# Kernel tuning notes

Measured on AMD Instinct MI355X. Metric: run time of the kernel, lower is better.

Reference implementation:

```python
import jax, jax.numpy as jnp
import numpy as np

HIDDEN = 2048
INTER = 4096
HEADS = 32
HEAD_DIM = INTER // HEADS  # 128
STATE = 128
GROUPS = 1
CONV_K = 4
CHUNK = 256
EPS = 1e-5
CONV_DIM = INTER + 2 * GROUPS * STATE  # 4352
DT_MIN, DT_MAX = 0.0, 100.0
BATCH, SEQ = 2, 4096


def _segment_sum(x):
    """Stable segment sum: returns (..., T, T) with entry [i,j] = sum_{k=j+1..i} x[k] (-inf above diag)."""
    T = x.shape[-1]
    xx = jnp.broadcast_to(x[..., None], x.shape + (T,))
    mask_lower = jnp.tril(jnp.ones((T, T), bool), -1)
    xx = jnp.where(mask_lower, xx, 0.0)
    seg = jnp.cumsum(xx, axis=-2)
    mask_incl = jnp.tril(jnp.ones((T, T), bool), 0)
    return jnp.where(mask_incl, seg, -jnp.inf)


def setup_inputs() -> dict:
    key = jax.random.key(0)
    ks = jax.random.split(key, 8)
    std = 0.02
    return {
        "hidden_states": jax.random.normal(ks[0], (BATCH, SEQ, HIDDEN), jnp.float32),
        "in_proj_w": jax.random.normal(ks[1], (INTER + CONV_DIM + HEADS, HIDDEN), jnp.float32) * std,
        "conv_w": jax.random.normal(ks[2], (CONV_DIM, 1, CONV_K), jnp.float32) * std,
        "conv_b": jnp.zeros((CONV_DIM,), jnp.float32),
        "A_log": jnp.log(jax.random.uniform(ks[3], (HEADS,), jnp.float32, 1.0, 16.0)),
        "dt_bias": jax.random.normal(ks[4], (HEADS,), jnp.float32) * 0.1,
        "D": jnp.ones((HEADS,), jnp.float32),
        "norm_w": jnp.ones((INTER,), jnp.float32),
        "out_proj_w": jax.random.normal(ks[5], (HIDDEN, INTER), jnp.float32) * (std / np.sqrt(48.0)),
    }


def reference(hidden_states, in_proj_w, conv_w, conv_b, A_log, dt_bias, D, norm_w, out_proj_w):
    b, s, _ = hidden_states.shape
    # in_proj and split into gate / conv-input / dt
    proj = hidden_states @ in_proj_w.T
    gate, hBC, dt = jnp.split(proj, [INTER, INTER + CONV_DIM], axis=-1)

    # causal depthwise conv1d (padding k-1 left, truncate to seq_len) + SiLU
    x = jnp.transpose(hBC, (0, 2, 1))  # (b, conv_dim, s)
    x = jax.lax.conv_general_dilated(
        x, conv_w, window_strides=(1,), padding=[(CONV_K - 1, 0)],
        dimension_numbers=("NCH", "OIH", "NCH"), feature_group_count=CONV_DIM)
    x = x + conv_b[None, :, None]
    hBC = jax.nn.silu(jnp.transpose(x, (0, 2, 1)))  # (b, s, conv_dim)

    xs, B, C = jnp.split(hBC, [INTER, INTER + GROUPS * STATE], axis=-1)

    A = -jnp.exp(A_log)  # (h,)
    dt = jnp.clip(jax.nn.softplus(dt + dt_bias), DT_MIN, DT_MAX)  # (b, s, h)

    xs = xs.reshape(b, s, HEADS, HEAD_DIM)
    rep = HEADS // GROUPS
    Bm = jnp.repeat(B.reshape(b, s, GROUPS, STATE), rep, axis=2)  # (b,s,h,n)
    Cm = jnp.repeat(C.reshape(b, s, GROUPS, STATE), rep, axis=2)

    pad = (-s) % CHUNK

    def padseq(t):
        return jnp.pad(t, ((0, 0), (0, pad)) + ((0, 0),) * (t.ndim - 2))

    D_res = D[None, None, :, None] * padseq(xs)  # (b, S, h, p)
    xdt = padseq(xs * dt[..., None])
    Ad = padseq(A[None, None, :] * dt)  # (b, S, h)
    Bm, Cm = padseq(Bm), padseq(Cm)

    nc = (s + pad) // CHUNK
    xdt = xdt.reshape(b, nc, CHUNK, HEADS, HEAD_DIM)
    Ad = jnp.transpose(Ad.reshape(b, nc, CHUNK, HEADS), (0, 3, 1, 2))  # (b,h,c,l)
    Bm = Bm.reshape(b, nc, CHUNK, HEADS, STATE)
    Cm = Cm.reshape(b, nc, CHUNK, HEADS, STATE)

    A_cum = jnp.cumsum(Ad, axis=-1)  # (b,h,c,l)

    # 1) intra-chunk (diagonal block) output
    L = jnp.exp(_segment_sum(Ad))  # (b,h,c,l,l)
    G = jnp.einsum("bclhn,bcshn->bclsh", Cm, Bm)
    M = G * jnp.transpose(L, (0, 2, 3, 4, 1))
    Y_diag = jnp.einsum("bclsh,bcshp->bclhp", M, xdt)

    # 2) per-chunk final states
    decay_states = jnp.exp(A_cum[:, :, :, -1:] - A_cum)  # (b,h,c,l)
    B_decay = Bm * jnp.transpose(decay_states, (0, 2, 3, 1))[..., None]
    states = jnp.einsum("bclhn,bclhp->bchpn", B_decay, xdt)  # (b,c,h,p,n)

    # 3) inter-chunk recurrence
    states = jnp.concatenate([jnp.zeros_like(states[:, :1]), states], axis=1)  # (b,c+1,h,p,n)
    chunk_sums = jnp.pad(A_cum[:, :, :, -1], ((0, 0), (0, 0), (1, 0)))  # (b,h,c+1)
    decay_chunk = jnp.exp(_segment_sum(chunk_sums))  # (b,h,c+1,c+1)
    decay_chunk = jnp.transpose(decay_chunk, (0, 2, 3, 1))  # (b,c,z,h)
    new_states = jnp.einsum("bczh,bchpn->bzhpn", decay_chunk, states)
    states = new_states[:, :-1]  # (b,c,h,p,n) state entering each chunk

    # 4) state -> output contribution
    state_decay = jnp.exp(A_cum)  # (b,h,c,l)
    Y_off = jnp.einsum("bclhn,bchpn->bclhp", Cm, states) * jnp.transpose(state_decay, (0, 2, 3, 1))[..., None]

    y = (Y_diag + Y_off).reshape(b, nc * CHUNK, HEADS, HEAD_DIM) + D_res
    y = y[:, :s].reshape(b, s, INTER)

    # gated RMSNorm
    y = y * jax.nn.silu(gate)
    var = jnp.mean(y * y, axis=-1, keepdims=True)
    y = y * jax.lax.rsqrt(var + EPS) * norm_w

    return y @ out_proj_w.T
```

## Files before the change

### kernel.cpp

```cpp
#include <hip/hip_runtime.h>

#define SEQ     4096
#define BATCH   2
#define NROWS   8192
#define HID     2048
#define INTER_  4096
#define NHEADS  32
#define HDIM    128
#define NSTATE  128
#define CDIM    4352
#define NPROJ_  8480
#define NPAD    8704
#define NCH     16
#define CHUNK_  256

typedef __attribute__((ext_vector_type(8))) short bf16x8;
typedef __attribute__((ext_vector_type(4))) short short4v;
typedef __attribute__((ext_vector_type(4))) float f32x4;

#define AS1 __attribute__((address_space(1)))
#define AS3 __attribute__((address_space(3)))

__device__ __forceinline__ float bf2f(short s) {
  union { unsigned u; float f; } x;
  x.u = ((unsigned)(unsigned short)s) << 16;
  return x.f;
}
__device__ __forceinline__ short f2bf(float f) {
  union { float f; unsigned u; } x; x.f = f;
  unsigned r = x.u + 0x7FFFu + ((x.u >> 16) & 1u);
  return (short)(r >> 16);
}

__global__ void cvt_bf16(const float* __restrict__ in, short* __restrict__ out,
                         int n4, int nsrc4) {
  int i = blockIdx.x * 256 + threadIdx.x;
  if (i >= n4) return;
  short4v o = {0, 0, 0, 0};
  if (i < nsrc4) {
    f32x4 v = *(const f32x4*)(in + (size_t)i * 4);
    o = (short4v){ f2bf(v.x), f2bf(v.y), f2bf(v.z), f2bf(v.w) };
  }
  *(short4v*)(out + (size_t)i * 4) = o;
}

template<int MODE>
__global__ __launch_bounds__(512, 1)
void gemm256(const short* __restrict__ A, const short* __restrict__ Bw,
             int M, int N, int K, int nM,
             float* __restrict__ outF, short* __restrict__ gate,
             short* __restrict__ hbc, float* __restrict__ dtraw)
{
  __shared__ __align__(16) short lds[2][2][2][256 * 32];
  const int tid = threadIdx.x;
  const int lane = tid & 63, wave = tid >> 6;
  const int l16 = lane & 15, lhi = lane >> 4;
  const int wm = wave >> 2, wn = wave & 3;

  const int bm = blockIdx.x % nM, bn = blockIdx.x / nM;
  const size_t row0 = (size_t)bm * 256;
  const int    col0 = bn * 256;

  const short* Ab  = A + row0 * K;
  const short* Bbp = Bw + (size_t)col0 * K;

  f32x4 acc[8][4];
  #pragma unroll
  for (int m = 0; m < 8; ++m)
    #pragma unroll
    for (int n = 0; n < 4; ++n) acc[m][n] = (f32x4){0.f, 0.f, 0.f, 0.f};

  auto stage = [&](int bufq, int mat, int kh, int ko) {
    const short* gsrc = mat ? Bbp : Ab;
    short* base = &lds[bufq][mat][kh][0];
    #pragma unroll
    for (int j = 0; j < 2; ++j) {
      int u = j * 512 + tid;
      int r = u >> 2;
      int g = (u & 3) ^ ((r >> 1) & 3);
      __builtin_amdgcn_global_load_lds(
          (const AS1 unsigned*)(gsrc + (size_t)r * K + ko + kh * 32 + g * 8),
          (AS3 unsigned*)(base + (j * 512 + wave * 64) * 8), 16, 0, 0);
    }
  };
  auto readA = [&](int bufq, int kh, int mh, bf16x8* a) {
    const short* base = &lds[bufq][0][kh][0];
    #pragma unroll
    for (int f = 0; f < 4; ++f) {
      int rr = wm * 128 + mh * 64 + f * 16 + l16;
      int g = lhi ^ ((rr >> 1) & 3);
      a[f] = *(const bf16x8*)(base + rr * 32 + g * 8);
    }
  };
  auto readB = [&](int bufq, int kh, bf16x8* b) {
    const short* base = &lds[bufq][1][kh][0];
    #pragma unroll
    for (int f = 0; f < 4; ++f) {
      int rr = wn * 64 + f * 16 + l16;
      int g = lhi ^ ((rr >> 1) & 3);
      b[f] = *(const bf16x8*)(base + rr * 32 + g * 8);
    }
  };

  const int nt = K / 64;
  stage(0, 0, 0, 0); stage(0, 1, 0, 0); stage(0, 0, 1, 0); stage(0, 1, 1, 0);

  for (int t = 0; t < nt; ++t) {
    const int buf = t & 1, nb = buf ^ 1;
    const int kon = (t + 1) * 64;
    const bool pf = (t + 1 < nt);

    if (pf) { stage(nb, 0, 0, kon); stage(nb, 1, 0, kon);
              stage(nb, 0, 1, kon); stage(nb, 1, 1, kon); }
    if (pf) asm volatile("s_waitcnt vmcnt(8)" ::: "memory");
    else    asm volatile("s_waitcnt vmcnt(0)" ::: "memory");
    __builtin_amdgcn_s_barrier();

    #pragma unroll
    for (int kh = 0; kh < 2; ++kh) {
      bf16x8 a[8], b[4];
      readA(buf, kh, 0, a); readA(buf, kh, 1, a + 4); readB(buf, kh, b);
      __builtin_amdgcn_s_setprio(1);
      #pragma unroll
      for (int mf = 0; mf < 8; ++mf)
        #pragma unroll
        for (int nf = 0; nf < 4; ++nf)
          acc[mf][nf] = __builtin_amdgcn_mfma_f32_16x16x32_bf16(a[mf], b[nf], acc[mf][nf], 0, 0, 0);
      __builtin_amdgcn_s_setprio(0);
    }
    __builtin_amdgcn_s_barrier();
  }

  #pragma unroll
  for (int mh = 0; mh < 2; ++mh) {
    #pragma unroll
    for (int f = 0; f < 4; ++f) {
      #pragma unroll
      for (int nf = 0; nf < 4; ++nf) {
        #pragma unroll
        for (int j = 0; j < 4; ++j) {
          int gr = (int)row0 + wm * 128 + mh * 64 + f * 16 + lhi * 4 + j;
          int gc = col0 + wn * 64 + nf * 16 + l16;
          float v = acc[mh * 4 + f][nf][j];
          if (MODE == 0) {
            outF[(size_t)gr * N + gc] = v;
          } else {
            if (gc < INTER_)             gate[(size_t)gr * INTER_ + gc] = f2bf(v);
            else if (gc < INTER_ + CDIM) hbc[(size_t)gr * CDIM + (gc - INTER_)] = f2bf(v);
            else if (gc < NPROJ_)        dtraw[(size_t)gr * NHEADS + (gc - INTER_ - CDIM)] = v;
          }
        }
      }
    }
  }
}

__global__ __launch_bounds__(256)
void conv_t(const short* __restrict__ hbc, const float* __restrict__ cw,
            const float* __restrict__ cb, short* __restrict__ xsT,
            short* __restrict__ Bb, short* __restrict__ Cb, short* __restrict__ BbT)
{
  __shared__ short sOut[64][130];
  int ct = blockIdx.y;
  int cl = threadIdx.x & 127;
  int rh = threadIdx.x >> 7;
  int c = ct * 128 + cl;
  int row0 = blockIdx.x * 64;
  int s0 = row0 & (SEQ - 1);
  float w0 = cw[c * 4 + 0], w1 = cw[c * 4 + 1], w2 = cw[c * 4 + 2], w3 = cw[c * 4 + 3];
  float bias = cb[c];
  int r0 = rh * 32;
  float h0, h1, h2;
  h0 = (s0 + r0 - 3 >= 0) ? bf2f(hbc[(size_t)(row0 + r0 - 3) * CDIM + c]) : 0.f;
  h1 = (s0 + r0 - 2 >= 0) ? bf2f(hbc[(size_t)(row0 + r0 - 2) * CDIM + c]) : 0.f;
  h2 = (s0 + r0 - 1 >= 0) ? bf2f(hbc[(size_t)(row0 + r0 - 1) * CDIM + c]) : 0.f;

  for (int r = r0; r < r0 + 32; ++r) {
    float xin = bf2f(hbc[(size_t)(row0 + r) * CDIM + c]);
    float a = bias + w0 * h0 + w1 * h1 + w2 * h2 + w3 * xin;
    h0 = h1; h1 = h2; h2 = xin;
    float v = a / (1.f + expf(-a));
    short bv = f2bf(v);
    if (ct < 33) sOut[r][cl] = bv;
    if (ct == 32)      Bb[(size_t)(row0 + r) * NSTATE + cl] = bv;
    else if (ct == 33) Cb[(size_t)(row0 + r) * NSTATE + cl] = bv;
  }
  if (ct >= 33) return;
  __syncthreads();
  int p = threadIdx.x >> 1, sh = (threadIdx.x & 1) * 32;
  int b = row0 >> 12;
  size_t dst;
  short* outp;
  if (ct < 32) { outp = xsT; dst = ((size_t)(b * 32 + ct) * 128 + p) * SEQ + s0 + sh; }
  else         { outp = BbT; dst = ((size_t)b * 128 + p) * SEQ + s0 + sh; }
  #pragma unroll
  for (int g = 0; g < 8; ++g) {
    short4v o;
    o[0] = sOut[sh + g * 4 + 0][p];
    o[1] = sOut[sh + g * 4 + 1][p];
    o[2] = sOut[sh + g * 4 + 2][p];
    o[3] = sOut[sh + g * 4 + 3][p];
    *(short4v*)(outp + dst + g * 4) = o;
  }
}

__global__ void dt_proc(const float* __restrict__ dtraw, const float* __restrict__ dtb,
                        float* __restrict__ dtT, int n) {
  int i = blockIdx.x * 256 + threadIdx.x;
  if (i >= n) return;
  float x = dtraw[i] + dtb[i & (NHEADS - 1)];
  float sp = (x > 20.f) ? x : log1pf(expf(x));
  float d = fminf(fmaxf(sp, 0.f), 100.f);
  int row = i >> 5, h = i & 31;
  dtT[(size_t)h * NROWS + row] = d;
}

__global__ __launch_bounds__(256)
void ssm_state(const short* __restrict__ xsT, const short* __restrict__ BbT,
               const float* __restrict__ dtT, const float* __restrict__ Alog,
               short* __restrict__ csb, float* __restrict__ dAsum)
{
  int blk = blockIdx.x;
  int h = blk & 31, cc = (blk >> 5) & 15, b = blk >> 9;
  int tid = threadIdx.x, lane = tid & 63, wave = tid >> 6;
  int l16 = lane & 15, lhi = lane >> 4;
  int s0 = cc * CHUNK_;

  __shared__ float acum[256];
  __shared__ float sdt[256];
  { float Ah = -expf(Alog[h]);
    float d = dtT[(size_t)h * NROWS + (size_t)b * SEQ + s0 + tid];
    sdt[tid] = d; acum[tid] = Ah * d; }
  for (int off = 1; off < 256; off <<= 1) {
    __syncthreads();
    float v = (tid >= off) ? acum[tid - off] : 0.f;
    __syncthreads();
    acum[tid] += v;
  }
  __syncthreads();
  float alast = acum[255];

  const short* xbase = xsT + ((size_t)(b * 32 + h) * 128) * SEQ + s0;
  const short* bbase = BbT + ((size_t)b * 128) * SEQ + s0;

  f32x4 acc[2][8];
  #pragma unroll
  for (int m = 0; m < 2; ++m)
    #pragma unroll
    for (int n = 0; n < 8; ++n) acc[m][n] = (f32x4){0.f, 0.f, 0.f, 0.f};

  for (int lt0 = 0; lt0 < 256; lt0 += 32) {
    float fe[8];
    #pragma unroll
    for (int e = 0; e < 8; ++e) {
      int kl = lt0 + lhi * 8 + e;
      fe[e] = sdt[kl] * __expf(alast - acum[kl]);
    }
    bf16x8 af[2];
    #pragma unroll
    for (int m = 0; m < 2; ++m) {
      bf16x8 raw = *(const bf16x8*)(xbase + (size_t)(wave * 32 + m * 16 + l16) * SEQ + lt0 + lhi * 8);
      bf16x8 sc;
      #pragma unroll
      for (int e = 0; e < 8; ++e) sc[e] = f2bf(bf2f(raw[e]) * fe[e]);
      af[m] = sc;
    }
    #pragma unroll
    for (int n = 0; n < 8; ++n) {
      bf16x8 bfv = *(const bf16x8*)(bbase + (size_t)(n * 16 + l16) * SEQ + lt0 + lhi * 8);
      acc[0][n] = __builtin_amdgcn_mfma_f32_16x16x32_bf16(af[0], bfv, acc[0][n], 0, 0, 0);
      acc[1][n] = __builtin_amdgcn_mfma_f32_16x16x32_bf16(af[1], bfv, acc[1][n], 0, 0, 0);
    }
  }
  size_t base = (size_t)blk * 16384;
  #pragma unroll
  for (int m = 0; m < 2; ++m)
    #pragma unroll
    for (int n = 0; n < 8; ++n)
      #pragma unroll
      for (int j = 0; j < 4; ++j) {
        int p = wave * 32 + m * 16 + lhi * 4 + j;
        int ng = n * 16 + l16;
        csb[base + (size_t)p * NSTATE + ng] = f2bf(acc[m][n][j]);
      }
  if (tid == 0) dAsum[blk] = alast;
}

__global__ void ssm_scan(short* __restrict__ csb, const float* __restrict__ dAsum) {
  int idx = blockIdx.x * 256 + threadIdx.x;
  int np = idx & 16383;
  int bh = idx >> 14;
  int h = bh & 31, b = bh >> 5;
  float run = 0.f;
  #pragma unroll
  for (int c = 0; c < NCH; ++c) {
    size_t base = ((size_t)((b * NCH + c) * NHEADS + h)) * 16384 + np;
    float v = bf2f(csb[base]);
    csb[base] = f2bf(run);
    run = run * __expf(dAsum[(b * NCH + c) * NHEADS + h]) + v;
  }
}

__global__ __launch_bounds__(256)
void ssm_y(const short* __restrict__ xsT, const short* __restrict__ Bb,
           const short* __restrict__ Cb, const float* __restrict__ dtT,
           const float* __restrict__ Alog, const float* __restrict__ Dv,
           const short* __restrict__ csb, short* __restrict__ gateY)
{
  int blk = blockIdx.y, lt = blockIdx.x;
  int h = blk & 31, cc = (blk >> 5) & 15, b = blk >> 9;
  int tid = threadIdx.x, lane = tid & 63, wave = tid >> 6;
  int l16 = lane & 15, lhi = lane >> 4;
  int s0 = cc * CHUNK_;
  size_t row0 = (size_t)b * SEQ + s0;

  __shared__ float acum[256];
  __shared__ float sdt[256];
  __shared__ __align__(16) short M_lds[64 * 264];

  { float Ah = -expf(Alog[h]);
    float d = dtT[(size_t)h * NROWS + row0 + tid];
    sdt[tid] = d; acum[tid] = Ah * d; }
  for (int off = 1; off < 256; off <<= 1) {
    __syncthreads();
    float v = (tid >= off) ? acum[tid - off] : 0.f;
    __syncthreads();
    acum[tid] += v;
  }
  __syncthreads();

  float Dh = Dv[h];

  {
    f32x4 acc1[4][4];
    #pragma unroll
    for (int m = 0; m < 4; ++m)
      #pragma unroll
      for (int n = 0; n < 4; ++n) acc1[m][n] = (f32x4){0.f, 0.f, 0.f, 0.f};
    for (int kk = 0; kk < NSTATE; kk += 32) {
      bf16x8 af[4], bv[4];
      #pragma unroll
      for (int m = 0; m < 4; ++m)
        af[m] = *(const bf16x8*)(Cb + (row0 + lt * 64 + m * 16 + l16) * NSTATE + kk + lhi * 8);
      #pragma unroll
      for (int n = 0; n < 4; ++n)
        bv[n] = *(const bf16x8*)(Bb + (row0 + wave * 64 + n * 16 + l16) * NSTATE + kk + lhi * 8);
      #pragma unroll
      for (int m = 0; m < 4; ++m)
        #pragma unroll
        for (int n = 0; n < 4; ++n)
          acc1[m][n] = __builtin_amdgcn_mfma_f32_16x16x32_bf16(af[m], bv[n], acc1[m][n], 0, 0, 0);
    }
    float as_[4]; int sg_[4];
    #pragma unroll
    for (int n = 0; n < 4; ++n) { sg_[n] = wave * 64 + n * 16 + l16; as_[n] = acum[sg_[n]]; }
    #pragma unroll
    for (int m = 0; m < 4; ++m) {
      #pragma unroll
      for (int j = 0; j < 4; ++j) {
        int ll = m * 16 + lhi * 4 + j;
        int lg = lt * 64 + ll;
        float al = acum[lg];
        float dinv = Dh / fmaxf(sdt[lg], 1e-20f);
        #pragma unroll
        for (int n = 0; n < 4; ++n) {
          float v = 0.f;
          if (sg_[n] <= lg) {
            v = acc1[m][n][j] * __expf(al - as_[n]);
            if (sg_[n] == lg) v += dinv;
          }
          M_lds[ll * 264 + wave * 64 + n * 16 + l16] = f2bf(v);
        }
      }
    }
  }
  __syncthreads();

  const short* xbase = xsT + ((size_t)(b * 32 + h) * 128) * SEQ + s0;

  f32x4 accY[4][2];
  #pragma unroll
  for (int m = 0; m < 4; ++m) { accY[m][0] = (f32x4){0,0,0,0}; accY[m][1] = (f32x4){0,0,0,0}; }
  int smax = (lt + 1) * 64;
  for (int st = 0; st < smax; st += 32) {
    float fe[8];
    #pragma unroll
    for (int e = 0; e < 8; ++e) fe[e] = sdt[st + lhi * 8 + e];
    bf16x8 bv2[2];
    #pragma unroll
    for (int n = 0; n < 2; ++n) {
      bf16x8 raw = *(const bf16x8*)(xbase + (size_t)(wave * 32 + n * 16 + l16) * SEQ + st + lhi * 8);
      bf16x8 sc;
      #pragma unroll
      for (int e = 0; e < 8; ++e) sc[e] = f2bf(bf2f(raw[e]) * fe[e]);
      bv2[n] = sc;
    }
    #pragma unroll
    for (int m = 0; m < 4; ++m) {
      bf16x8 a = *(const bf16x8*)(M_lds + (m * 16 + l16) * 264 + st + lhi * 8);
      accY[m][0] = __builtin_amdgcn_mfma_f32_16x16x32_bf16(a, bv2[0], accY[m][0], 0, 0, 0);
      accY[m][1] = __builtin_amdgcn_mfma_f32_16x16x32_bf16(a, bv2[1], accY[m][1], 0, 0, 0);
    }
  }

  f32x4 accO[4][2];
  #pragma unroll
  for (int m = 0; m < 4; ++m) { accO[m][0] = (f32x4){0,0,0,0}; accO[m][1] = (f32x4){0,0,0,0}; }
  const short* sbase = csb + (size_t)blk * 16384;
  for (int nt = 0; nt < NSTATE; nt += 32) {
    bf16x8 bv2[2];
    #pragma unroll
    for (int n = 0; n < 2; ++n) {
      int p = wave * 32 + n * 16 + l16;
      bv2[n] = *(const bf16x8*)(sbase + (size_t)p * NSTATE + nt + lhi * 8);
    }
    #pragma unroll
    for (int m = 0; m < 4; ++m) {
      bf16x8 a = *(const bf16x8*)(Cb + (row0 + lt * 64 + m * 16 + l16) * NSTATE + nt + lhi * 8);
      accO[m][0] = __builtin_amdgcn_mfma_f32_16x16x32_bf16(a, bv2[0], accO[m][0], 0, 0, 0);
      accO[m][1] = __builtin_amdgcn_mfma_f32_16x16x32_bf16(a, bv2[1], accO[m][1], 0, 0, 0);
    }
  }

  #pragma unroll
  for (int m = 0; m < 4; ++m) {
    #pragma unroll
    for (int j = 0; j < 4; ++j) {
      int ll = m * 16 + lhi * 4 + j;
      float e = __expf(acum[lt * 64 + ll]);
      size_t row = row0 + lt * 64 + ll;
      #pragma unroll
      for (int n = 0; n < 2; ++n) {
        int p = wave * 32 + n * 16 + l16;
        size_t adr = row * INTER_ + h * HDIM + p;
        float yv = accY[m][n][j] + e * accO[m][n][j];
        float g = bf2f(gateY[adr]);
        gateY[adr] = f2bf(yv * g / (1.f + expf(-g)));
      }
    }
  }
}

__global__ __launch_bounds__(256)
void gate_norm(short* __restrict__ ybf, const float* __restrict__ nw)
{
  int row = blockIdx.x;
  int tid = threadIdx.x;
  size_t base = (size_t)row * INTER_;
  float vals[16];
  float ss = 0.f;
  #pragma unroll
  for (int i = 0; i < 16; ++i) {
    int idx = tid + i * 256;
    float v = bf2f(ybf[base + idx]);
    vals[i] = v;
    ss += v * v;
  }
  #pragma unroll
  for (int off = 32; off > 0; off >>= 1) ss += __shfl_down(ss, off);
  __shared__ float ws4[4];
  if ((tid & 63) == 0) ws4[tid >> 6] = ss;
  __syncthreads();
  float tot = ws4[0] + ws4[1] + ws4[2] + ws4[3];
  float scale = rsqrtf(tot * (1.f / 4096.f) + 1e-5f);
  #pragma unroll
  for (int i = 0; i < 16; ++i) {
    int idx = tid + i * 256;
    ybf[base + idx] = f2bf(vals[i] * scale * nw[idx]);
  }
}

extern "C" void kernel_launch(void* const* d_in, const int* in_sizes, int n_in,
                              void* d_out, int out_size, void* d_ws, size_t ws_size,
                              hipStream_t stream)
{
  const float* Xf   = (const float*)d_in[0];
  const float* W1f  = (const float*)d_in[1];
  const float* cw   = (const float*)d_in[2];
  const float* cb   = (const float*)d_in[3];
  const float* Alog = (const float*)d_in[4];
  const float* dtb  = (const float*)d_in[5];
  const float* Dv   = (const float*)d_in[6];
  const float* nw   = (const float*)d_in[7];
  const float* W2f  = (const float*)d_in[8];
  float* outp = (float*)d_out;
  char* ws = (char*)d_ws;

  size_t off = 0;
  short* Xb  = (short*)(ws + off); off += (size_t)NROWS * HID * 2;
  short* W1b = (short*)(ws + off); off += (size_t)NPAD * HID * 2;
  short* xsT = (short*)ws;
  short* W2b = (short*)(ws + off); off += (size_t)HID * INTER_ * 2;
  short* gateY = (short*)(ws + off); off += (size_t)NROWS * INTER_ * 2;
  short* hbc  = (short*)(ws + off); off += (size_t)NROWS * CDIM * 2;
  float* dtv  = (float*)(ws + off); off += (size_t)NROWS * NHEADS * 4;
  float* dtT  = (float*)(ws + off); off += (size_t)NROWS * NHEADS * 4;
  short* Bb   = (short*)(ws + off); off += (size_t)NROWS * NSTATE * 2;
  short* Cb   = (short*)(ws + off); off += (size_t)NROWS * NSTATE * 2;
  short* BbT  = (short*)(ws + off); off += (size_t)NROWS * NSTATE * 2;
  float* dAs  = (float*)(ws + off); off += 4096;
  short* csb  = (short*)hbc;

  cvt_bf16<<<(NROWS * HID / 4 + 255) / 256, 256, 0, stream>>>(
      Xf, Xb, NROWS * HID / 4, NROWS * HID / 4);
  cvt_bf16<<<(NPAD * HID / 4 + 255) / 256, 256, 0, stream>>>(
      W1f, W1b, NPAD * HID / 4, NPROJ_ * HID / 4);
  cvt_bf16<<<(HID * INTER_ / 4 + 255) / 256, 256, 0, stream>>>(
      W2f, W2b, HID * INTER_ / 4, HID * INTER_ / 4);

  gemm256<1><<<(NROWS / 256) * (NPAD / 256), 512, 0, stream>>>(
      Xb, W1b, NROWS, NPROJ_, HID, NROWS / 256, nullptr, gateY, hbc, dtv);

  dt_proc<<<(NROWS * NHEADS) / 256, 256, 0, stream>>>(dtv, dtb, dtT, NROWS * NHEADS);
  conv_t<<<dim3(NROWS / 64, 34), 256, 0, stream>>>(hbc, cw, cb, xsT, Bb, Cb, BbT);

  ssm_state<<<BATCH * NCH * NHEADS, 256, 0, stream>>>(xsT, BbT, dtT, Alog, csb, dAs);
  ssm_scan<<<(BATCH * NHEADS * 16384) / 256, 256, 0, stream>>>(csb, dAs);
  ssm_y<<<dim3(4, BATCH * NCH * NHEADS), 256, 0, stream>>>(xsT, Bb, Cb, dtT, Alog, Dv, csb, gateY);

  gate_norm<<<NROWS, 256, 0, stream>>>(gateY, nw);

  gemm256<0><<<(NROWS / 256) * (HID / 256), 512, 0, stream>>>(
      gateY, W2b, NROWS, HID, INTER_, NROWS / 256, outp, nullptr, nullptr, nullptr);
}
```

Measured before the change: 926.6 us.

## Split GEMM k-tile waits per half and fuse dt softplus into epilogue

The bf16 GEMM main loop now issues next-tile prefetches inside the first k-half and waits for and synchronises on each k-half separately. Compute on the first half of a tile can then start before the second half has arrived, with an extra barrier per iteration as the cost. Separately, the dt bias add, softplus and clamp are moved into the in-projection GEMM epilogue, which writes the transposed dtT directly. This removes the dt_proc launch and its intermediate buffer, at the price of transcendental work in a few epilogue lanes.

```diff
diff --git a/kernel.cpp b/kernel.cpp
--- a/kernel.cpp
+++ b/kernel.cpp
@@ -49,7 +49,8 @@
 void gemm256(const short* __restrict__ A, const short* __restrict__ Bw,
              int M, int N, int K, int nM,
              float* __restrict__ outF, short* __restrict__ gate,
-             short* __restrict__ hbc, float* __restrict__ dtraw)
+             short* __restrict__ hbc, float* __restrict__ dtT,
+             const float* __restrict__ dtb)
 {
   __shared__ __align__(16) short lds[2][2][2][256 * 32];
   const int tid = threadIdx.x;
@@ -104,20 +105,20 @@
 
   const int nt = K / 64;
   stage(0, 0, 0, 0); stage(0, 1, 0, 0); stage(0, 0, 1, 0); stage(0, 1, 1, 0);
+  asm volatile("s_waitcnt vmcnt(4)" ::: "memory");
+  __builtin_amdgcn_s_barrier();
 
   for (int t = 0; t < nt; ++t) {
     const int buf = t & 1, nb = buf ^ 1;
     const int kon = (t + 1) * 64;
     const bool pf = (t + 1 < nt);
 
-    if (pf) { stage(nb, 0, 0, kon); stage(nb, 1, 0, kon);
-              stage(nb, 0, 1, kon); stage(nb, 1, 1, kon); }
-    if (pf) asm volatile("s_waitcnt vmcnt(8)" ::: "memory");
-    else    asm volatile("s_waitcnt vmcnt(0)" ::: "memory");
-    __builtin_amdgcn_s_barrier();
-
     #pragma unroll
     for (int kh = 0; kh < 2; ++kh) {
+      if (pf && kh == 0) {
+        stage(nb, 0, 0, kon); stage(nb, 1, 0, kon);
+        stage(nb, 0, 1, kon); stage(nb, 1, 1, kon);
+      }
       bf16x8 a[8], b[4];
       readA(buf, kh, 0, a); readA(buf, kh, 1, a + 4); readB(buf, kh, b);
       __builtin_amdgcn_s_setprio(1);
@@ -127,8 +128,15 @@
         for (int nf = 0; nf < 4; ++nf)
           acc[mf][nf] = __builtin_amdgcn_mfma_f32_16x16x32_bf16(a[mf], b[nf], acc[mf][nf], 0, 0, 0);
       __builtin_amdgcn_s_setprio(0);
-    }
-    __builtin_amdgcn_s_barrier();
+      if (kh == 0) {
+        if (pf) asm volatile("s_waitcnt vmcnt(8)" ::: "memory");
+        else    asm volatile("s_waitcnt vmcnt(0)" ::: "memory");
+        __builtin_amdgcn_s_barrier();
+      } else if (pf) {
+        asm volatile("s_waitcnt vmcnt(4)" ::: "memory");
+        __builtin_amdgcn_s_barrier();
+      }
+    }
   }
 
   #pragma unroll
@@ -147,7 +155,12 @@
           } else {
             if (gc < INTER_)             gate[(size_t)gr * INTER_ + gc] = f2bf(v);
             else if (gc < INTER_ + CDIM) hbc[(size_t)gr * CDIM + (gc - INTER_)] = f2bf(v);
-            else if (gc < NPROJ_)        dtraw[(size_t)gr * NHEADS + (gc - INTER_ - CDIM)] = v;
+            else if (gc < NPROJ_) {
+              int h = gc - INTER_ - CDIM;
+              float x = v + dtb[h];
+              float sp = (x > 20.f) ? x : log1pf(expf(x));
+              dtT[(size_t)h * NROWS + gr] = fminf(fmaxf(sp, 0.f), 100.f);
+            }
           }
         }
       }
@@ -204,17 +217,6 @@
   }
 }
 
-__global__ void dt_proc(const float* __restrict__ dtraw, const float* __restrict__ dtb,
-                        float* __restrict__ dtT, int n) {
-  int i = blockIdx.x * 256 + threadIdx.x;
-  if (i >= n) return;
-  float x = dtraw[i] + dtb[i & (NHEADS - 1)];
-  float sp = (x > 20.f) ? x : log1pf(expf(x));
-  float d = fminf(fmaxf(sp, 0.f), 100.f);
-  int row = i >> 5, h = i & 31;
-  dtT[(size_t)h * NROWS + row] = d;
-}
-
 __global__ __launch_bounds__(256)
 void ssm_state(const short* __restrict__ xsT, const short* __restrict__ BbT,
                const float* __restrict__ dtT, const float* __restrict__ Alog,
@@ -493,7 +495,6 @@
   short* W2b = (short*)(ws + off); off += (size_t)HID * INTER_ * 2;
   short* gateY = (short*)(ws + off); off += (size_t)NROWS * INTER_ * 2;
   short* hbc  = (short*)(ws + off); off += (size_t)NROWS * CDIM * 2;
-  float* dtv  = (float*)(ws + off); off += (size_t)NROWS * NHEADS * 4;
   float* dtT  = (float*)(ws + off); off += (size_t)NROWS * NHEADS * 4;
   short* Bb   = (short*)(ws + off); off += (size_t)NROWS * NSTATE * 2;
   short* Cb   = (short*)(ws + off); off += (size_t)NROWS * NSTATE * 2;
@@ -509,9 +510,8 @@
       W2f, W2b, HID * INTER_ / 4, HID * INTER_ / 4);
 
   gemm256<1><<<(NROWS / 256) * (NPAD / 256), 512, 0, stream>>>(
-      Xb, W1b, NROWS, NPROJ_, HID, NROWS / 256, nullptr, gateY, hbc, dtv);
-
-  dt_proc<<<(NROWS * NHEADS) / 256, 256, 0, stream>>>(dtv, dtb, dtT, NROWS * NHEADS);
+      Xb, W1b, NROWS, NPROJ_, HID, NROWS / 256, nullptr, gateY, hbc, dtT, dtb);
+
   conv_t<<<dim3(NROWS / 64, 34), 256, 0, stream>>>(hbc, cw, cb, xsT, Bb, Cb, BbT);
 
   ssm_state<<<BATCH * NCH * NHEADS, 256, 0, stream>>>(xsT, BbT, dtT, Alog, csb, dAs);
@@ -521,5 +521,5 @@
   gate_norm<<<NROWS, 256, 0, stream>>>(gateY, nw);
 
   gemm256<0><<<(NROWS / 256) * (HID / 256), 512, 0, stream>>>(
-      gateY, W2b, NROWS, HID, INTER_, NROWS / 256, outp, nullptr, nullptr, nullptr);
-}
+      gateY, W2b, NROWS, HID, INTER_, NROWS / 256, outp, nullptr, nullptr, nullptr, nullptr);
+}
```

After: 969.7 us. +4.7%, slower.
